# Kernel tuning notes

Measured on AMD Instinct MI355X. Metric: run time of the kernel, lower is better.

Reference implementation:

```python
import jax, jax.numpy as jnp
import numpy as np

COMMITMENT_COST = 0.25


def setup_inputs() -> dict:
    key = jax.random.key(0)
    k1, k2 = jax.random.split(key)
    z = jax.random.normal(k1, (32, 256, 32, 32), dtype=jnp.float32)
    # Embedding init mirrors uniform(-1/codebook_size, 1/codebook_size)
    emb = jax.random.uniform(k2, (4096, 256), dtype=jnp.float32,
                             minval=-1.0 / 4096, maxval=1.0 / 4096)
    return {"z": z, "emb": emb}


def reference(z, emb):
    # z: [b, c, h, w] with c == token_size; emb: [codebook_size, token_size]
    b, c, h, w = z.shape
    z_bhwc = jnp.transpose(z, (0, 2, 3, 1))           # [b, h, w, c]
    z_flat = z_bhwc.reshape(-1, c)                    # [N, c]

    # Squared-distance matrix: ||z||^2 + ||e||^2 - 2 z e^T  -> [N, K]
    d = (jnp.sum(z_flat * z_flat, axis=1, keepdims=True)
         + jnp.sum(emb * emb, axis=1)
         - 2.0 * jnp.einsum('nd,kd->nk', z_flat, emb))

    idx = jnp.argmin(d, axis=1)                       # [N]
    z_q = emb[idx].reshape(z_bhwc.shape)              # [b, h, w, c]

    commitment_loss = COMMITMENT_COST * jnp.mean(
        (jax.lax.stop_gradient(z_q) - z_bhwc) ** 2)
    codebook_loss = jnp.mean((z_q - jax.lax.stop_gradient(z_bhwc)) ** 2)
    loss = commitment_loss + codebook_loss

    # Straight-through estimator
    z_q = z_bhwc + jax.lax.stop_gradient(z_q - z_bhwc)
    z_q = jnp.transpose(z_q, (0, 3, 1, 2))            # [b, c, h, w]

    min_encoding_indices = idx.reshape(b, h, w)
    return z_q, loss, commitment_loss, codebook_loss, min_encoding_indices
```

## Files before the change

kernel.cpp:

```cpp
#include <hip/hip_runtime.h>

#define CDIM 256
#define CB   4096
#define HW   1024
#define NTOK 32768
#define NELEM 8388608
#define MARGIN 3.5e-4f
#define OVCAP 64

typedef float f32x4 __attribute__((ext_vector_type(4)));
typedef short bf16x8 __attribute__((ext_vector_type(8)));
typedef unsigned int u32;
typedef unsigned long long u64;

__device__ __forceinline__ unsigned short f2bf(float x) {
    u32 b = __float_as_uint(x);
    return (unsigned short)((b + 0x7fffu + ((b >> 16) & 1u)) >> 16);
}
__device__ __forceinline__ u32 fenc(float f) {
    u32 b = __float_as_uint(f);
    return (b & 0x80000000u) ? ~b : (b | 0x80000000u);
}
__device__ __forceinline__ float fdec(u32 u) {
    return __uint_as_float((u & 0x80000000u) ? (u & 0x7fffffffu) : ~u);
}
__device__ __forceinline__ u64 shfl_xor_u64(u64 v, int s) {
    u32 lo = __shfl_xor((u32)v, s);
    u32 hi = __shfl_xor((u32)(v >> 32), s);
    return ((u64)hi << 32) | lo;
}
__device__ __forceinline__ void gl_lds16(const void* g, void* l) {
    __builtin_amdgcn_global_load_lds(
        (const __attribute__((address_space(1))) u32*)g,
        (__attribute__((address_space(3))) u32*)l, 16, 0, 0);
}


__global__ __launch_bounds__(1024) void prep(const float* __restrict__ z,
                                             const float* __restrict__ emb,
                                             float* __restrict__ zT,
                                             unsigned short* __restrict__ z_hip,
                                             float* __restrict__ zn,
                                             u32* __restrict__ ovcnt,
                                             float* __restrict__ enorm2,
                                             unsigned short* __restrict__ e_hip,
                                             u32* __restrict__ cnt2) {
    __shared__ float T[128][128];
    const int tid = threadIdx.x;
    const int rg = blockIdx.x;
    if (tid < 32) {
        const int code = rg * 16 + (tid >> 1);
        const int cl = code & 127;
        const int cgE = code >> 7;
        const int sxzE = (cl >> 1) & 3;
        float s = 0.f;
#pragma unroll
        for (int kb = 0; kb < 4; ++kb) {
            const int c0 = (tid & 1) * 128 + kb * 32;
            const int kc = c0 >> 5;
            __align__(16) unsigned short tmp[32];
#pragma unroll
            for (int q = 0; q < 8; ++q) {
                float4 v = *(const float4*)(emb + (size_t)code * CDIM + c0 + 4 * q);
                s += v.x * v.x + v.y * v.y + v.z * v.z + v.w * v.w;
                tmp[4 * q + 0] = f2bf(v.x); tmp[4 * q + 1] = f2bf(v.y);
                tmp[4 * q + 2] = f2bf(v.z); tmp[4 * q + 3] = f2bf(v.w);
            }
            uint4* dst4 = (uint4*)(e_hip + (((size_t)(cgE * 8 + kc) * 128 + cl) * 32));
#pragma unroll
            for (int q = 0; q < 4; ++q)
                dst4[q ^ sxzE] = *(uint4*)&tmp[8 * q];
        }
        s += __shfl_xor(s, 1);
        if ((tid & 1) == 0) enorm2[code] = s;
        if (rg == 0 && tid == 0) *cnt2 = 0u;
    }
    const int b = rg >> 3, hw0 = (rg * 128) & 1023;
    const float* zb = z + (size_t)b * (CDIM * HW) + hw0;
    const int tt = tid & 127;
    const int kcl = (tid >> 7) & 3;
    const int hbit = tid >> 9;
    const int hof = hbit * 16;
    const int q0 = hbit * 2;
    const int sxz = (tt >> 1) & 3;
    float zacc = 0.f;
#pragma unroll
    for (int grp = 0; grp < 2; ++grp) {
        const int c0 = grp * 128;
        __syncthreads();
#pragma unroll
        for (int p = 0; p < 16; ++p) {
            const int c = p * 8 + (tid >> 7);
            T[c][tid & 127] = zb[(size_t)(c0 + c) * HW + (tid & 127)];
        }
        __syncthreads();
        const int kc = grp * 4 + kcl;
        const int cb = kcl * 32 + hof;
        float* dstT = zT + (size_t)(rg * 128 + tt) * CDIM + c0 + cb;
        __align__(16) unsigned short us[16];
#pragma unroll
        for (int q = 0; q < 4; ++q) {
            float4 v;
            v.x = T[cb + 4 * q + 0][tt]; v.y = T[cb + 4 * q + 1][tt];
            v.z = T[cb + 4 * q + 2][tt]; v.w = T[cb + 4 * q + 3][tt];
            ((float4*)dstT)[q] = v;
            zacc += v.x * v.x + v.y * v.y + v.z * v.z + v.w * v.w;
            us[4 * q + 0] = f2bf(v.x); us[4 * q + 1] = f2bf(v.y);
            us[4 * q + 2] = f2bf(v.z); us[4 * q + 3] = f2bf(v.w);
        }
        uint4* d4 = (uint4*)(z_hip + (((size_t)(rg * 8 + kc) * 128 + tt) * 32));
        d4[q0 ^ sxz]       = *(uint4*)&us[0];
        d4[(q0 + 1) ^ sxz] = *(uint4*)&us[8];
    }
    __syncthreads();
    float* zp = &T[0][0];
    zp[(tid >> 7) * 128 + tt] = zacc;
    __syncthreads();
    if (tid < 128) {
        float s = 0.f;
#pragma unroll
        for (int r = 0; r < 8; ++r) s += zp[r * 128 + tid];
        zn[rg * 128 + tid] = s;
        ovcnt[rg * 128 + tid] = 0u;
    }
}


__global__ __launch_bounds__(256, 4) void p1(const unsigned short* __restrict__ z_hip,
                                             const unsigned short* __restrict__ e_hip,
                                             const float* __restrict__ enorm2,
                                             u64* __restrict__ cand,
                                             u32* __restrict__ ovcnt,
                                             u64* __restrict__ ovslot) {
    __shared__ __align__(16) unsigned short Bs[2][128 * 32];
    const int bid = blockIdx.x;
    const int rg = bid >> 5, cg = bid & 31;
    const int tid = threadIdx.x;
    const int w = tid >> 6, lane = tid & 63;
    const int quad = lane >> 4, l15 = lane & 15;
    const int swz = (quad ^ ((l15 >> 1) & 3)) * 8;

    f32x4 acc[2][8];
#pragma unroll
    for (int i = 0; i < 2; ++i)
#pragma unroll
        for (int j = 0; j < 8; ++j)
#pragma unroll
            for (int e = 0; e < 4; ++e) acc[i][j][e] = 0.f;

    const char* gB = (const char*)e_hip + ((size_t)cg << 16) + w * 2048 + lane * 16;
    const char* gA0 = (const char*)z_hip + ((size_t)rg << 16)
                      + (w * 32 + l15) * 64 + swz * 2;
    char* lB = (char*)Bs + w * 2048;
    gl_lds16(gB, lB);           gl_lds16(gB + 1024, lB + 1024);
    gB += 8192;
    bf16x8 af0 = *(const bf16x8*)(gA0);
    bf16x8 af1 = *(const bf16x8*)(gA0 + 1024);
    __syncthreads();
#pragma unroll
    for (int kc = 0; kc < 8; ++kc) {
        const int cur = kc & 1;
        bf16x8 afn0, afn1;
        if (kc < 7) {
            char* dB = lB + (cur ^ 1) * 8192;
            gl_lds16(gB, dB);       gl_lds16(gB + 1024, dB + 1024);
            gB += 8192;
            asm volatile("" ::: "memory");
            const char* gA = gA0 + (size_t)(kc + 1) * 8192;
            afn0 = *(const bf16x8*)(gA);
            afn1 = *(const bf16x8*)(gA + 1024);
        }
        const unsigned short* B0 = Bs[cur];
        __builtin_amdgcn_s_setprio(1);
#pragma unroll
        for (int nh = 0; nh < 2; ++nh) {
            bf16x8 bfr[4];
#pragma unroll
            for (int nj = 0; nj < 4; ++nj)
                bfr[nj] = *(const bf16x8*)&B0[((nh * 4 + nj) * 16 + l15) * 32 + swz];
#pragma unroll
            for (int nj = 0; nj < 4; ++nj) {
                acc[0][nh * 4 + nj] = __builtin_amdgcn_mfma_f32_16x16x32_bf16(
                    af0, bfr[nj], acc[0][nh * 4 + nj], 0, 0, 0);
                acc[1][nh * 4 + nj] = __builtin_amdgcn_mfma_f32_16x16x32_bf16(
                    af1, bfr[nj], acc[1][nh * 4 + nj], 0, 0, 0);
            }
        }
        __builtin_amdgcn_s_setprio(0);
        if (kc < 7) {
            af0 = afn0; af1 = afn1;
            asm volatile("s_waitcnt vmcnt(2)" ::: "memory");
            __builtin_amdgcn_s_barrier();
            asm volatile("" ::: "memory");
        }
    }
    float en[8];
#pragma unroll
    for (int ni = 0; ni < 8; ++ni) en[ni] = enorm2[cg * 128 + ni * 16 + l15];
#pragma unroll
    for (int mi = 0; mi < 2; ++mi) {
#pragma unroll
        for (int r = 0; r < 4; ++r) {
            const int row = w * 32 + mi * 16 + quad * 4 + r;
            const int t = rg * 128 + row;
            float dv[8];
#pragma unroll
            for (int ni = 0; ni < 8; ++ni) dv[ni] = en[ni] - 2.0f * acc[mi][ni][r];
            float m = fminf(fminf(fminf(dv[0], dv[1]), fminf(dv[2], dv[3])),
                            fminf(fminf(dv[4], dv[5]), fminf(dv[6], dv[7])));
            m = fminf(m, __shfl_xor(m, 1));
            m = fminf(m, __shfl_xor(m, 2));
            m = fminf(m, __shfl_xor(m, 4));
            m = fminf(m, __shfl_xor(m, 8));
            u32 myni = 8u;
#pragma unroll
            for (int ni = 7; ni >= 0; --ni)
                if (dv[ni] == m) myni = (u32)ni;
            const unsigned long long bal = __ballot(myni < 8u);
            const int sl = __ffs((u32)((bal >> (quad << 4)) & 0xFFFFu)) - 1;
            if (l15 == sl) {
                const u32 k = (u32)(cg * 128 + (int)myni * 16 + l15);
                cand[((size_t)t << 5) + cg] = ((u64)fenc(m) << 32) | k;
            }
            const float thr = m + MARGIN;
#pragma unroll
            for (int ni = 0; ni < 8; ++ni) {
                if (dv[ni] <= thr && !(l15 == sl && ni == (int)myni)) {
                    const u32 k = (u32)(cg * 128 + ni * 16 + l15);
                    const u32 pos = atomicAdd(&ovcnt[t], 1u);
                    if (pos < (u32)OVCAP)
                        ovslot[(size_t)t * OVCAP + pos] = ((u64)fenc(dv[ni]) << 32) | k;
                }
            }
        }
    }
}

__global__ __launch_bounds__(256) void k5(const float* __restrict__ zT,
                                          const float* __restrict__ emb,
                                          const float* __restrict__ enorm2,
                                          const float* __restrict__ zn,
                                          const u64* __restrict__ cand,
                                          const u32* __restrict__ ovcnt,
                                          const u64* __restrict__ ovslot,
                                          float* __restrict__ idxf,
                                          float* __restrict__ dmin) {
    const int t = (blockIdx.x * 256 + threadIdx.x) >> 6;
    const int lane = threadIdx.x & 63;
    const u64 pkv = cand[((size_t)t << 5) + (lane & 31)];
    u64 g = pkv;
#pragma unroll
    for (int s = 1; s < 32; s <<= 1) {
        const u64 o = shfl_xor_u64(g, s);
        g = o < g ? o : g;
    }
    const float thr = fdec((u32)(g >> 32)) + MARGIN;
    const float4 za = ((const float4*)(zT + (size_t)t * CDIM))[lane];
    const float znv = zn[t];
    float bdv = 1e30f; int bk = 0x7fffffff;
    unsigned long long q = __ballot(fdec((u32)(pkv >> 32)) <= thr)
                           & 0xFFFFFFFFull;
    while (q) {
        const int i = __ffsll(q) - 1; q &= q - 1;
        const int k = __shfl((int)(u32)pkv, i);
        const float4 ea = ((const float4*)(emb + (size_t)k * CDIM))[lane];
        float p = za.x * ea.x + za.y * ea.y + za.z * ea.z + za.w * ea.w;
#pragma unroll
        for (int s = 1; s < 64; s <<= 1) p += __shfl_xor(p, s);
        const float t1 = znv + enorm2[k];
        const float d = t1 - 2.0f * p;
        if (d < bdv || (d == bdv && k < bk)) { bdv = d; bk = k; }
    }
    u32 n = ovcnt[t]; if (n > (u32)OVCAP) n = (u32)OVCAP;
    for (u32 i = 0; i < n; ++i) {
        const u64 ov = ovslot[(size_t)t * OVCAP + i];
        if (!(fdec((u32)(ov >> 32)) <= thr)) continue;
        const int k = (int)(u32)ov;
        const float4 ea = ((const float4*)(emb + (size_t)k * CDIM))[lane];
        float p = za.x * ea.x + za.y * ea.y + za.z * ea.z + za.w * ea.w;
#pragma unroll
        for (int s = 1; s < 64; s <<= 1) p += __shfl_xor(p, s);
        const float t1 = znv + enorm2[k];
        const float d = t1 - 2.0f * p;
        if (d < bdv || (d == bdv && k < bk)) { bdv = d; bk = k; }
    }
    if (lane == 0) {
        idxf[t] = (float)bk;
        dmin[t] = bdv;
    }
}

__global__ __launch_bounds__(1024) void k2(const float* __restrict__ emb,
                                           const float* __restrict__ idxf,
                                           const float* __restrict__ dmin,
                                           float* __restrict__ zq,
                                           float* __restrict__ out3,
                                           u32* __restrict__ cnt2) {
    __shared__ int ks[64];
    __shared__ float red[1024];
    __shared__ int lastFlag;
    const int tid = threadIdx.x;
    const int tok0 = blockIdx.x * 64;
    const int b = tok0 >> 10, hw0 = tok0 & 1023;
    if (tid < 64) ks[tid] = (int)idxf[tok0 + tid];
    __syncthreads();
    const int t4 = (tid & 15) * 4;
    const int ka = ks[t4], kb = ks[t4 + 1], kc = ks[t4 + 2], kd = ks[t4 + 3];
    float* outb = zq + (size_t)b * (CDIM * HW) + hw0 + t4;
    int c = tid >> 4;
#pragma unroll
    for (int p = 0; p < 4; ++p, c += 64) {
        float4 v;
        v.x = emb[(size_t)ka * CDIM + c];
        v.y = emb[(size_t)kb * CDIM + c];
        v.z = emb[(size_t)kc * CDIM + c];
        v.w = emb[(size_t)kd * CDIM + c];
        *(float4*)(outb + (size_t)c * HW) = v;
    }
    if (tid == 0) lastFlag = (atomicAdd(cnt2, 1u) == 511u) ? 1 : 0;
    __syncthreads();
    if (lastFlag) {
        const float4* d4 = (const float4*)dmin;
        float s = 0.f;
        for (int i = tid; i < NTOK / 4; i += 1024) {
            const float4 v = d4[i];
            s += (v.x + v.y) + (v.z + v.w);
        }
        red[tid] = s;
        __syncthreads();
        for (int o = 512; o > 0; o >>= 1) {
            if (tid < o) red[tid] += red[tid + o];
            __syncthreads();
        }
        if (tid == 0) {
            const float mse = red[0] / (float)NELEM;
            out3[0] = 1.25f * mse;
            out3[1] = 0.25f * mse;
            out3[2] = mse;
        }
    }
}

extern "C" void kernel_launch(void* const* d_in, const int* in_sizes, int n_in,
                              void* d_out, int out_size, void* d_ws, size_t ws_size,
                              hipStream_t stream) {
    const float* z   = (const float*)d_in[0];
    const float* emb = (const float*)d_in[1];
    float* out = (float*)d_out;
    char* w = (char*)d_ws;

    float* zn     = (float*)w;                       w += NTOK * 4;
    float* enorm2 = (float*)w;                       w += CB * 4;
    u32*   ovcnt  = (u32*)w;                         w += NTOK * 4;
    float* dmin   = (float*)w;                       w += NTOK * 4;
    u32*   cnt2   = (u32*)w;                         w += 256;
    float* zT     = (float*)w;                       w += (size_t)NTOK * CDIM * 4;
    unsigned short* z_hip = (unsigned short*)w;      w += (size_t)NTOK * CDIM * 2;
    unsigned short* e_hip = (unsigned short*)w;      w += (size_t)CB * CDIM * 2;
    u64*   cand   = (u64*)w;                         w += (size_t)NTOK * 32 * 8;
    u64*   ovslot = (u64*)w;                         w += (size_t)NTOK * OVCAP * 8;
    float* idxf = out + NELEM + 3;

    hipLaunchKernelGGL(prep, dim3(256),       dim3(1024), 0, stream,
                       z, emb, zT, z_hip, zn, ovcnt, enorm2, e_hip, cnt2);
    hipLaunchKernelGGL(p1,  dim3((NTOK / 128) * (CB / 128)), dim3(256), 0, stream,
                       z_hip, e_hip, enorm2, cand, ovcnt, ovslot);
    hipLaunchKernelGGL(k5,  dim3(NTOK / 4),   dim3(256), 0, stream,
                       zT, emb, enorm2, zn, cand, ovcnt, ovslot, idxf, dmin);
    hipLaunchKernelGGL(k2,  dim3(NTOK / 64),  dim3(1024), 0, stream,
                       emb, idxf, dmin, out, out + NELEM, cnt2);
}
```

Before: 257.8 us.

## Fuse refinement and gather kernels, remap blocks per XCD, gate overflow atomics

Merges the candidate-refinement kernel and the gather/loss kernel into one launch. Each 1024-thread block now refines 64 tokens and then writes their quantized vectors straight from shared memory, which removes a launch and the idxf round trip. The GEMM kernel remaps block IDs so that each XCD gets a contiguous range of row groups, aiming for better L2 reuse of z tiles. It also adds a wave ballot that skips the overflow-atomic loop when no lane in the quad has extra near-minimum candidates. Thread fences are added so the last block reads dmin correctly.

```diff
diff --git a/kernel.cpp b/kernel.cpp
--- a/kernel.cpp
+++ b/kernel.cpp
@@ -134,7 +134,10 @@
                                              u64* __restrict__ ovslot) {
     __shared__ __align__(16) unsigned short Bs[2][128 * 32];
     const int bid = blockIdx.x;
-    const int rg = bid >> 5, cg = bid & 31;
+    const int xcd = bid & 7;
+    const int seq = bid >> 3;
+    const int rg = xcd * 32 + (seq >> 5);
+    const int cg = seq & 31;
     const int tid = threadIdx.x;
     const int w = tid >> 6, lane = tid & 63;
     const int quad = lane >> 4, l15 = lane & 15;
@@ -223,87 +226,92 @@
                 cand[((size_t)t << 5) + cg] = ((u64)fenc(m) << 32) | k;
             }
             const float thr = m + MARGIN;
-#pragma unroll
-            for (int ni = 0; ni < 8; ++ni) {
-                if (dv[ni] <= thr && !(l15 == sl && ni == (int)myni)) {
-                    const u32 k = (u32)(cg * 128 + ni * 16 + l15);
-                    const u32 pos = atomicAdd(&ovcnt[t], 1u);
-                    if (pos < (u32)OVCAP)
-                        ovslot[(size_t)t * OVCAP + pos] = ((u64)fenc(dv[ni]) << 32) | k;
+            int cnt = 0;
+#pragma unroll
+            for (int ni = 0; ni < 8; ++ni) cnt += (dv[ni] <= thr) ? 1 : 0;
+            const unsigned long long ob =
+                __ballot(cnt > ((l15 == sl) ? 1 : 0));
+            if ((ob >> (quad << 4)) & 0xFFFFull) {
+#pragma unroll
+                for (int ni = 0; ni < 8; ++ni) {
+                    if (dv[ni] <= thr && !(l15 == sl && ni == (int)myni)) {
+                        const u32 k = (u32)(cg * 128 + ni * 16 + l15);
+                        const u32 pos = atomicAdd(&ovcnt[t], 1u);
+                        if (pos < (u32)OVCAP)
+                            ovslot[(size_t)t * OVCAP + pos] =
+                                ((u64)fenc(dv[ni]) << 32) | k;
+                    }
                 }
             }
         }
     }
 }
 
-__global__ __launch_bounds__(256) void k5(const float* __restrict__ zT,
-                                          const float* __restrict__ emb,
-                                          const float* __restrict__ enorm2,
-                                          const float* __restrict__ zn,
-                                          const u64* __restrict__ cand,
-                                          const u32* __restrict__ ovcnt,
-                                          const u64* __restrict__ ovslot,
-                                          float* __restrict__ idxf,
-                                          float* __restrict__ dmin) {
-    const int t = (blockIdx.x * 256 + threadIdx.x) >> 6;
-    const int lane = threadIdx.x & 63;
-    const u64 pkv = cand[((size_t)t << 5) + (lane & 31)];
-    u64 g = pkv;
-#pragma unroll
-    for (int s = 1; s < 32; s <<= 1) {
-        const u64 o = shfl_xor_u64(g, s);
-        g = o < g ? o : g;
-    }
-    const float thr = fdec((u32)(g >> 32)) + MARGIN;
-    const float4 za = ((const float4*)(zT + (size_t)t * CDIM))[lane];
-    const float znv = zn[t];
-    float bdv = 1e30f; int bk = 0x7fffffff;
-    unsigned long long q = __ballot(fdec((u32)(pkv >> 32)) <= thr)
-                           & 0xFFFFFFFFull;
-    while (q) {
-        const int i = __ffsll(q) - 1; q &= q - 1;
-        const int k = __shfl((int)(u32)pkv, i);
-        const float4 ea = ((const float4*)(emb + (size_t)k * CDIM))[lane];
-        float p = za.x * ea.x + za.y * ea.y + za.z * ea.z + za.w * ea.w;
-#pragma unroll
-        for (int s = 1; s < 64; s <<= 1) p += __shfl_xor(p, s);
-        const float t1 = znv + enorm2[k];
-        const float d = t1 - 2.0f * p;
-        if (d < bdv || (d == bdv && k < bk)) { bdv = d; bk = k; }
-    }
-    u32 n = ovcnt[t]; if (n > (u32)OVCAP) n = (u32)OVCAP;
-    for (u32 i = 0; i < n; ++i) {
-        const u64 ov = ovslot[(size_t)t * OVCAP + i];
-        if (!(fdec((u32)(ov >> 32)) <= thr)) continue;
-        const int k = (int)(u32)ov;
-        const float4 ea = ((const float4*)(emb + (size_t)k * CDIM))[lane];
-        float p = za.x * ea.x + za.y * ea.y + za.z * ea.z + za.w * ea.w;
-#pragma unroll
-        for (int s = 1; s < 64; s <<= 1) p += __shfl_xor(p, s);
-        const float t1 = znv + enorm2[k];
-        const float d = t1 - 2.0f * p;
-        if (d < bdv || (d == bdv && k < bk)) { bdv = d; bk = k; }
-    }
-    if (lane == 0) {
-        idxf[t] = (float)bk;
-        dmin[t] = bdv;
-    }
-}
-
-__global__ __launch_bounds__(1024) void k2(const float* __restrict__ emb,
-                                           const float* __restrict__ idxf,
-                                           const float* __restrict__ dmin,
-                                           float* __restrict__ zq,
-                                           float* __restrict__ out3,
-                                           u32* __restrict__ cnt2) {
+__global__ __launch_bounds__(1024) void k52(const float* __restrict__ zT,
+                                            const float* __restrict__ emb,
+                                            const float* __restrict__ enorm2,
+                                            const float* __restrict__ zn,
+                                            const u64* __restrict__ cand,
+                                            const u32* __restrict__ ovcnt,
+                                            const u64* __restrict__ ovslot,
+                                            float* __restrict__ idxf,
+                                            float* __restrict__ dmin,
+                                            float* __restrict__ zq,
+                                            float* __restrict__ out3,
+                                            u32* __restrict__ cnt2) {
     __shared__ int ks[64];
     __shared__ float red[1024];
     __shared__ int lastFlag;
     const int tid = threadIdx.x;
     const int tok0 = blockIdx.x * 64;
+    const int wv = tid >> 6, lane = tid & 63;
+    for (int j = 0; j < 4; ++j) {
+        const int t = tok0 + wv * 4 + j;
+        const u64 pkv = cand[((size_t)t << 5) + (lane & 31)];
+        u64 g = pkv;
+#pragma unroll
+        for (int s = 1; s < 32; s <<= 1) {
+            const u64 o = shfl_xor_u64(g, s);
+            g = o < g ? o : g;
+        }
+        const float thr = fdec((u32)(g >> 32)) + MARGIN;
+        const float4 za = ((const float4*)(zT + (size_t)t * CDIM))[lane];
+        const float znv = zn[t];
+        float bdv = 1e30f; int bk = 0x7fffffff;
+        unsigned long long q = __ballot(fdec((u32)(pkv >> 32)) <= thr)
+                               & 0xFFFFFFFFull;
+        while (q) {
+            const int i = __ffsll(q) - 1; q &= q - 1;
+            const int k = __shfl((int)(u32)pkv, i);
+            const float4 ea = ((const float4*)(emb + (size_t)k * CDIM))[lane];
+            float p = za.x * ea.x + za.y * ea.y + za.z * ea.z + za.w * ea.w;
+#pragma unroll
+            for (int s = 1; s < 64; s <<= 1) p += __shfl_xor(p, s);
+            const float t1 = znv + enorm2[k];
+            const float d = t1 - 2.0f * p;
+            if (d < bdv || (d == bdv && k < bk)) { bdv = d; bk = k; }
+        }
+        u32 n = ovcnt[t]; if (n > (u32)OVCAP) n = (u32)OVCAP;
+        for (u32 i = 0; i < n; ++i) {
+            const u64 ov = ovslot[(size_t)t * OVCAP + i];
+            if (!(fdec((u32)(ov >> 32)) <= thr)) continue;
+            const int k = (int)(u32)ov;
+            const float4 ea = ((const float4*)(emb + (size_t)k * CDIM))[lane];
+            float p = za.x * ea.x + za.y * ea.y + za.z * ea.z + za.w * ea.w;
+#pragma unroll
+            for (int s = 1; s < 64; s <<= 1) p += __shfl_xor(p, s);
+            const float t1 = znv + enorm2[k];
+            const float d = t1 - 2.0f * p;
+            if (d < bdv || (d == bdv && k < bk)) { bdv = d; bk = k; }
+        }
+        if (lane == 0) {
+            ks[wv * 4 + j] = bk;
+            idxf[t] = (float)bk;
+            dmin[t] = bdv;
+        }
+    }
+    __syncthreads();
     const int b = tok0 >> 10, hw0 = tok0 & 1023;
-    if (tid < 64) ks[tid] = (int)idxf[tok0 + tid];
-    __syncthreads();
     const int t4 = (tid & 15) * 4;
     const int ka = ks[t4], kb = ks[t4 + 1], kc = ks[t4 + 2], kd = ks[t4 + 3];
     float* outb = zq + (size_t)b * (CDIM * HW) + hw0 + t4;
@@ -317,9 +325,11 @@
         v.w = emb[(size_t)kd * CDIM + c];
         *(float4*)(outb + (size_t)c * HW) = v;
     }
+    __threadfence();
     if (tid == 0) lastFlag = (atomicAdd(cnt2, 1u) == 511u) ? 1 : 0;
     __syncthreads();
     if (lastFlag) {
+        __threadfence();
         const float4* d4 = (const float4*)dmin;
         float s = 0.f;
         for (int i = tid; i < NTOK / 4; i += 1024) {
@@ -365,8 +375,7 @@
                        z, emb, zT, z_hip, zn, ovcnt, enorm2, e_hip, cnt2);
     hipLaunchKernelGGL(p1,  dim3((NTOK / 128) * (CB / 128)), dim3(256), 0, stream,
                        z_hip, e_hip, enorm2, cand, ovcnt, ovslot);
-    hipLaunchKernelGGL(k5,  dim3(NTOK / 4),   dim3(256), 0, stream,
-                       zT, emb, enorm2, zn, cand, ovcnt, ovslot, idxf, dmin);
-    hipLaunchKernelGGL(k2,  dim3(NTOK / 64),  dim3(1024), 0, stream,
-                       emb, idxf, dmin, out, out + NELEM, cnt2);
-}
+    hipLaunchKernelGGL(k52, dim3(NTOK / 64),  dim3(1024), 0, stream,
+                       zT, emb, enorm2, zn, cand, ovcnt, ovslot, idxf, dmin,
+                       out, out + NELEM, cnt2);
+}
```

Result: slower. 481.4 us (+86.7%).
